# Kernel tuning notes

Hardware: AMD Instinct MI355X
Metric: run time of the kernel (lower is better)

## Reference

```python
import jax, jax.numpy as jnp
import numpy as np
import math

HIDDEN = 2048
HEADS = 16
GROUPS = 4
HEAD_DIM = HIDDEN // HEADS  # 128
KV_DIM = GROUPS * HEAD_DIM  # 512
B, S = 2, 2048


def setup_inputs() -> dict:
    key = jax.random.key(0)
    ks = jax.random.split(key, 10)
    scale = 0.02
    return {
        "X": jax.random.normal(ks[0], (B, S, HIDDEN), dtype=jnp.float32),
        "attention_mask": jnp.ones((B, S), dtype=jnp.int32),
        "Wq": jax.random.normal(ks[1], (HIDDEN, HIDDEN), dtype=jnp.float32) * scale,
        "bq": jnp.zeros((HIDDEN,), dtype=jnp.float32),
        "Wk": jax.random.normal(ks[2], (HIDDEN, KV_DIM), dtype=jnp.float32) * scale,
        "bk": jnp.zeros((KV_DIM,), dtype=jnp.float32),
        "Wv": jax.random.normal(ks[3], (HIDDEN, KV_DIM), dtype=jnp.float32) * scale,
        "bv": jnp.zeros((KV_DIM,), dtype=jnp.float32),
        "Wo": jax.random.normal(ks[4], (HIDDEN, HIDDEN), dtype=jnp.float32) * scale,
        "bo": jnp.zeros((HIDDEN,), dtype=jnp.float32),
    }


def reference(X, attention_mask, Wq, bq, Wk, bk, Wv, bv, Wo, bo):
    b, s, _ = X.shape
    num_per_group = HEADS // GROUPS
    # projections
    Q = (X @ Wq + bq).reshape(b, s, HEADS, HEAD_DIM).transpose(0, 2, 1, 3)   # [b,H,s,d]
    K = (X @ Wk + bk).reshape(b, s, GROUPS, HEAD_DIM).transpose(0, 2, 1, 3)  # [b,G,s,d]
    V = (X @ Wv + bv).reshape(b, s, GROUPS, HEAD_DIM).transpose(0, 2, 1, 3)
    # torch .repeat(1, num_per_group, 1, 1) tiles group axis: [g0..gG-1, g0..gG-1, ...]
    K = jnp.tile(K, (1, num_per_group, 1, 1))  # [b,H,s,d]
    V = jnp.tile(V, (1, num_per_group, 1, 1))
    scores = jnp.einsum("bhqd,bhkd->bhqk", Q, K) / math.sqrt(HEAD_DIM)
    mask = attention_mask[:, None, None, :] == 0  # [b,1,1,s]
    scores = jnp.where(mask, jnp.float32(-jnp.inf), scores)
    attn = jax.nn.softmax(scores, axis=-1)
    out = jnp.einsum("bhqk,bhkd->bhqd", attn, V)  # [b,H,s,d]
    out = out.transpose(0, 2, 1, 3).reshape(b, s, HIDDEN)
    return out @ Wo + bo
```

## Files before the change

kernel.cpp:

```cpp
#include <hip/hip_runtime.h>
#include <hip/hip_bf16.h>


typedef __attribute__((ext_vector_type(8))) short short8;
typedef __attribute__((ext_vector_type(4))) short short4v;
typedef __attribute__((ext_vector_type(4))) float float4v;
typedef __attribute__((ext_vector_type(16))) float float16v;

#define C1F 0.12751743f
#define B0F -16.0f

#if defined(__has_builtin) && __has_builtin(__builtin_amdgcn_exp2f)
#define EXP2(x) __builtin_amdgcn_exp2f(x)
#else
#define EXP2(x) exp2f(x)
#endif

__device__ __forceinline__ short f2bf(float x) {
    __hip_bfloat16 h = __float2bfloat16(x);
    short s; __builtin_memcpy(&s, &h, sizeof(s)); return s;
}

__device__ __forceinline__ void gl16(const short* g, short* l) {
    __builtin_amdgcn_global_load_lds(
        (const __attribute__((address_space(1))) void*)g,
        (__attribute__((address_space(3))) void*)l, 16, 0, 0);
}

__global__ __launch_bounds__(256) void prep_kernel(
    const float* __restrict__ X, short* __restrict__ Xb,
    const float* __restrict__ Wq, const float* __restrict__ Wk,
    const float* __restrict__ Wv, const float* __restrict__ Wo,
    short* __restrict__ WqkvT, short* __restrict__ Wot) {
    __shared__ float tile[32][33];
    const int bxg = blockIdx.x;
    if (bxg < 8192) {
        int i = (bxg * 256 + threadIdx.x) * 4;
        float4 v = *(const float4*)(X + i);
        short4v o;
        o[0] = f2bf(v.x); o[1] = f2bf(v.y); o[2] = f2bf(v.z); o[3] = f2bf(v.w);
        *(short4v*)(Xb + i) = o;
        return;
    }
    const int tid = bxg - 8192;
    int bx = tid % 160;
    const int k0 = (tid / 160) * 32;
    const float* W; short* Wt; int N;
    if (bx < 64)      { W = Wq; Wt = WqkvT;                      N = 2048; }
    else if (bx < 80) { W = Wk; Wt = WqkvT + (size_t)2048 * 2048; N = 512; bx -= 64; }
    else if (bx < 96) { W = Wv; Wt = WqkvT + (size_t)2560 * 2048; N = 512; bx -= 80; }
    else              { W = Wo; Wt = Wot;                        N = 2048; bx -= 96; }
    const int K = 2048;
    const int n0 = bx * 32;
    const int tx = threadIdx.x & 31, ty = threadIdx.x >> 5;
#pragma unroll
    for (int i = 0; i < 4; ++i) {
        int kk = ty + i * 8;
        tile[kk][tx] = W[(size_t)(k0 + kk) * N + n0 + tx];
    }
    __syncthreads();
#pragma unroll
    for (int i = 0; i < 4; ++i) {
        int nn = ty + i * 8;
        Wt[(size_t)(n0 + nn) * K + k0 + tx] = f2bf(tile[tx][nn]);
    }
}

__global__ __launch_bounds__(256) void gemm_dma_kernel(
    const short* __restrict__ A, const short* __restrict__ Bt,
    const float* __restrict__ b0, const float* __restrict__ b1, const float* __restrict__ b2,
    short* __restrict__ O0, short* __restrict__ O1, short* __restrict__ O2,
    float* __restrict__ Of, int K, int mode) {
    __shared__ short As[128 * 64];
    __shared__ short Bs[128 * 64];
    const int t = threadIdx.x, lane = t & 63, w = t >> 6;
    const int l15 = lane & 15, quad = lane >> 4;
    const int wm = (w & 1) * 64, wn = (w >> 1) * 64;
    const int m0 = blockIdx.y * 128, n0 = blockIdx.x * 128;
    const int r8 = lane >> 3;
    const int csw = ((lane & 7) ^ r8) * 8;
    const short* ga = A + (size_t)(m0 + w * 8 + r8) * K + csw;
    const short* gb = Bt + (size_t)(n0 + w * 8 + r8) * K + csw;
    short* lA = As + (w * 8) * 64;
    short* lB = Bs + (w * 8) * 64;
    const int xs = l15 & 7;

    float4v acc[4][4] = {};

    for (int k0 = 0; k0 < K; k0 += 64) {
#pragma unroll
        for (int c = 0; c < 4; ++c) {
            gl16(ga + k0 + (size_t)(c * 32) * K, lA + c * 2048);
            gl16(gb + k0 + (size_t)(c * 32) * K, lB + c * 2048);
        }
        __syncthreads();
#pragma unroll
        for (int ks = 0; ks < 2; ++ks) {
            short8 af[4], bfr[4];
            const int ps = ((ks * 4 + quad) ^ xs) * 8;
#pragma unroll
            for (int i = 0; i < 4; ++i)
                af[i] = *(const short8*)(As + (wm + i * 16 + l15) * 64 + ps);
#pragma unroll
            for (int j = 0; j < 4; ++j)
                bfr[j] = *(const short8*)(Bs + (wn + j * 16 + l15) * 64 + ps);
#pragma unroll
            for (int i = 0; i < 4; ++i)
#pragma unroll
                for (int j = 0; j < 4; ++j)
                    acc[i][j] = __builtin_amdgcn_mfma_f32_16x16x32_bf16(af[i], bfr[j], acc[i][j], 0, 0, 0);
        }
        __syncthreads();
    }

#pragma unroll
    for (int i = 0; i < 4; ++i) {
#pragma unroll
        for (int j = 0; j < 4; ++j) {
            const int col = n0 + wn + j * 16 + l15;
            const int row0 = m0 + wm + i * 16 + quad * 4;
            if (mode == 1) {
                const float bc = b0[col];
#pragma unroll
                for (int r = 0; r < 4; ++r)
                    Of[(size_t)(row0 + r) * 2048 + col] = acc[i][j][r] + bc;
            } else if (col < 2048) {
                const float bc = b0[col];
#pragma unroll
                for (int r = 0; r < 4; ++r)
                    O0[(size_t)(row0 + r) * 2048 + col] = f2bf(acc[i][j][r] + bc);
            } else if (col < 2560) {
                const int c = col - 2048;
                const float bc = b1[c];
#pragma unroll
                for (int r = 0; r < 4; ++r)
                    O1[(size_t)(row0 + r) * 512 + c] = f2bf(acc[i][j][r] + bc);
            } else {
                const int c = col - 2560;
                const float bc = b2[c];
                const int qsw = ((quad & 1) << 1) | (quad >> 1);
                const int prow = m0 + wm + i * 16 + qsw * 4;
#pragma unroll
                for (int r = 0; r < 4; ++r)
                    O2[(size_t)c * 4096 + prow + r] = f2bf(acc[i][j][r] + bc);
            }
        }
    }
}

__global__ __launch_bounds__(256, 2) void flash_kernel(
    const short* __restrict__ Qb, const short* __restrict__ Kb,
    const short* __restrict__ Vt, const int* __restrict__ mask,
    short* __restrict__ Ab) {
    __shared__ short Ks[2][64 * 136];
    __shared__ short Vs[2][128 * 72];

    const int t = threadIdx.x;
    const int lane = t & 63, w = t >> 6;
    const int l31 = lane & 31, hi = lane >> 5;
    const int qt = blockIdx.x, g = blockIdx.y, b = blockIdx.z;
    const int h = g + 4 * w;
    const int q0 = qt * 32;

    short8 qf[8];
#pragma unroll
    for (int dd = 0; dd < 8; ++dd)
        qf[dd] = *(const short8*)(Qb + (size_t)(b * 2048 + q0 + l31) * 2048
                                  + h * 128 + dd * 16 + hi * 8);

    float16v o[4] = {};
    float rsum = 0.f;

    const int kR = t >> 4, kC = (t & 15) * 8;
    const int vR = t >> 3, vC = (t & 7) * 8;
    const short* kg = Kb + (size_t)(b * 2048 + kR) * 512 + g * 128 + kC;
    const short* vg = Vt + (size_t)(g * 128 + vR) * 4096 + (size_t)b * 2048 + vC;

    short8 kv[4], vv[4];
    int mvr = 1;

#define LOADT(KB)                                                                  \
    do {                                                                           \
        kv[0] = *(const short8*)(kg + (size_t)(KB) * 512);                         \
        kv[1] = *(const short8*)(kg + (size_t)((KB) + 16) * 512);                  \
        kv[2] = *(const short8*)(kg + (size_t)((KB) + 32) * 512);                  \
        kv[3] = *(const short8*)(kg + (size_t)((KB) + 48) * 512);                  \
        vv[0] = *(const short8*)(vg + (KB));                                       \
        vv[1] = *(const short8*)(vg + (size_t)32 * 4096 + (KB));                   \
        vv[2] = *(const short8*)(vg + (size_t)64 * 4096 + (KB));                   \
        vv[3] = *(const short8*)(vg + (size_t)96 * 4096 + (KB));                   \
        mvr = mask[b * 2048 + (KB) + lane];                                        \
    } while (0)

#define STAGE(BUF)                                                                 \
    do {                                                                           \
        _Pragma("unroll")                                                          \
        for (int i_ = 0; i_ < 4; ++i_)                                             \
            *(short8*)(&Ks[BUF][(kR + i_ * 16) * 136 + kC]) = kv[i_];              \
        _Pragma("unroll")                                                          \
        for (int i_ = 0; i_ < 4; ++i_)                                             \
            *(short8*)(&Vs[BUF][(vR + i_ * 32) * 72 + vC]) = vv[i_];               \
    } while (0)

    LOADT(0);
    STAGE(0);
    unsigned long long bits = __ballot(mvr != 0);
    LOADT(64);
    __syncthreads();

    int cur = 0;
    unsigned long long bits_next = bits;

    for (int kt = 0; kt < 32; ++kt) {
        if (kt + 1 < 32) {
            STAGE(cur ^ 1);
            bits_next = __ballot(mvr != 0);
            if (kt + 2 < 32) LOADT((kt + 2) * 64);
        }
        const short* Ksb = &Ks[cur][0];
        const short* Vsb = &Vs[cur][0];

        float16v st0 = {}, st1 = {};
        __builtin_amdgcn_s_setprio(1);
#pragma unroll
        for (int dd = 0; dd < 8; ++dd) {
            short8 kf0 = *(const short8*)(Ksb + l31 * 136 + dd * 16 + hi * 8);
            short8 kf1 = *(const short8*)(Ksb + (32 + l31) * 136 + dd * 16 + hi * 8);
            st0 = __builtin_amdgcn_mfma_f32_32x32x16_bf16(kf0, qf[dd], st0, 0, 0, 0);
            st1 = __builtin_amdgcn_mfma_f32_32x32x16_bf16(kf1, qf[dd], st1, 0, 0, 0);
        }
        __builtin_amdgcn_s_setprio(0);

        const bool full = (bits == ~0ull);
        const unsigned int mlo = ((unsigned int)bits) >> (4 * hi);
        const unsigned int mhi = ((unsigned int)(bits >> 32)) >> (4 * hi);

        if (full) {
#pragma unroll
            for (int e = 0; e < 16; ++e) {
                float p0 = EXP2(fmaf(st0[e], C1F, B0F));
                rsum += p0; st0[e] = p0;
            }
        } else {
#pragma unroll
            for (int e = 0; e < 16; ++e) {
                const int koff = (e & 3) + 8 * (e >> 2);
                float p0 = EXP2(fmaf(st0[e], C1F, B0F));
                p0 = ((mlo >> koff) & 1) ? p0 : 0.f;
                rsum += p0; st0[e] = p0;
            }
        }

        __builtin_amdgcn_s_setprio(1);
#pragma unroll
        for (int cc = 0; cc < 2; ++cc) {
            short8 pa;
#pragma unroll
            for (int e = 0; e < 8; ++e) pa[e] = f2bf(st0[cc * 8 + e]);
#pragma unroll
            for (int db = 0; db < 4; ++db) {
                short8 vb = *(const short8*)(Vsb + (db * 32 + l31) * 72 + cc * 16 + hi * 8);
                o[db] = __builtin_amdgcn_mfma_f32_32x32x16_bf16(pa, vb, o[db], 0, 0, 0);
            }
        }
        __builtin_amdgcn_s_setprio(0);

        if (full) {
#pragma unroll
            for (int e = 0; e < 16; ++e) {
                float p1 = EXP2(fmaf(st1[e], C1F, B0F));
                rsum += p1; st1[e] = p1;
            }
        } else {
#pragma unroll
            for (int e = 0; e < 16; ++e) {
                const int koff = (e & 3) + 8 * (e >> 2);
                float p1 = EXP2(fmaf(st1[e], C1F, B0F));
                p1 = ((mhi >> koff) & 1) ? p1 : 0.f;
                rsum += p1; st1[e] = p1;
            }
        }

        __builtin_amdgcn_s_setprio(1);
#pragma unroll
        for (int cc = 2; cc < 4; ++cc) {
            short8 pa;
#pragma unroll
            for (int e = 0; e < 8; ++e) pa[e] = f2bf(st1[(cc & 1) * 8 + e]);
#pragma unroll
            for (int db = 0; db < 4; ++db) {
                short8 vb = *(const short8*)(Vsb + (db * 32 + l31) * 72 + cc * 16 + hi * 8);
                o[db] = __builtin_amdgcn_mfma_f32_32x32x16_bf16(pa, vb, o[db], 0, 0, 0);
            }
        }
        __builtin_amdgcn_s_setprio(0);

        __syncthreads();
        bits = bits_next;
        cur ^= 1;
    }
#undef LOADT
#undef STAGE

    rsum += __shfl_xor(rsum, 32, 64);
    const float rinv = (rsum > 0.f) ? 1.f / rsum : 0.f;
    float rq[16];
#pragma unroll
    for (int e = 0; e < 16; ++e) {
        const int koff = (e & 3) + 8 * (e >> 2);
        rq[e] = __shfl(rinv, koff + 4 * hi, 64);
    }
    const size_t ob = (size_t)(b * 2048 + q0) * 2048 + h * 128;
#pragma unroll
    for (int db = 0; db < 4; ++db)
#pragma unroll
        for (int e = 0; e < 16; ++e) {
            const int koff = (e & 3) + 8 * (e >> 2);
            Ab[ob + (size_t)(koff + 4 * hi) * 2048 + db * 32 + l31] =
                f2bf(o[db][e] * rq[e]);
        }
}

extern "C" void kernel_launch(void* const* d_in, const int* in_sizes, int n_in,
                              void* d_out, int out_size, void* d_ws, size_t ws_size,
                              hipStream_t stream) {
    (void)in_sizes; (void)n_in; (void)out_size; (void)ws_size;
    const float* X  = (const float*)d_in[0];
    const int* mask = (const int*)d_in[1];
    const float* Wq = (const float*)d_in[2];
    const float* bq = (const float*)d_in[3];
    const float* Wk = (const float*)d_in[4];
    const float* bk = (const float*)d_in[5];
    const float* Wv = (const float*)d_in[6];
    const float* bv = (const float*)d_in[7];
    const float* Wo = (const float*)d_in[8];
    const float* bo = (const float*)d_in[9];
    float* out = (float*)d_out;

    char* ws = (char*)d_ws;
    short* Xb     = (short*)(ws + 0);
    short* WqkvT  = (short*)(ws + 16777216);
    short* Wot    = (short*)(ws + 29360128);
    short* Qb     = (short*)(ws + 37748736);
    short* Kb     = (short*)(ws + 54525952);
    short* Vt     = (short*)(ws + 58720256);
    short* Ab     = Xb;

    const int HID = 2048;

    prep_kernel<<<18432, 256, 0, stream>>>(X, Xb, Wq, Wk, Wv, Wo, WqkvT, Wot);

    gemm_dma_kernel<<<dim3(24, 32), 256, 0, stream>>>(
        Xb, WqkvT, bq, bk, bv, Qb, Kb, Vt, nullptr, HID, 0);

    flash_kernel<<<dim3(64, 4, 2), 256, 0, stream>>>(Qb, Kb, Vt, mask, Ab);

    gemm_dma_kernel<<<dim3(16, 32), 256, 0, stream>>>(
        Ab, Wot, bo, nullptr, nullptr, nullptr, nullptr, nullptr, out, HID, 1);
}
```

Measured before the change: 304.8 us.

## Split flash attention KV tiles across two wave groups with LDS merge

```diff
diff --git a/kernel.cpp b/kernel.cpp
--- a/kernel.cpp
+++ b/kernel.cpp
@@ -148,18 +148,21 @@
     }
 }
 
-__global__ __launch_bounds__(256, 2) void flash_kernel(
+__global__ __launch_bounds__(512, 4) void flash_kernel(
     const short* __restrict__ Qb, const short* __restrict__ Kb,
     const short* __restrict__ Vt, const int* __restrict__ mask,
     short* __restrict__ Ab) {
-    __shared__ short Ks[2][64 * 136];
-    __shared__ short Vs[2][128 * 72];
+    __shared__ __align__(16) char smem[71680];
+    short* KsBase = (short*)smem;
+    short* VsBase = (short*)(smem + 34816);
+    float* mg = (float*)smem;
 
     const int t = threadIdx.x;
     const int lane = t & 63, w = t >> 6;
     const int l31 = lane & 31, hi = lane >> 5;
+    const int ksp = w >> 2;
     const int qt = blockIdx.x, g = blockIdx.y, b = blockIdx.z;
-    const int h = g + 4 * w;
+    const int h = g + 4 * (w & 3);
     const int q0 = qt * 32;
 
     short8 qf[8];
@@ -176,30 +179,26 @@
     const short* kg = Kb + (size_t)(b * 2048 + kR) * 512 + g * 128 + kC;
     const short* vg = Vt + (size_t)(g * 128 + vR) * 4096 + (size_t)b * 2048 + vC;
 
-    short8 kv[4], vv[4];
+    short8 kv[2], vv[2];
     int mvr = 1;
 
 #define LOADT(KB)                                                                  \
     do {                                                                           \
         kv[0] = *(const short8*)(kg + (size_t)(KB) * 512);                         \
-        kv[1] = *(const short8*)(kg + (size_t)((KB) + 16) * 512);                  \
-        kv[2] = *(const short8*)(kg + (size_t)((KB) + 32) * 512);                  \
-        kv[3] = *(const short8*)(kg + (size_t)((KB) + 48) * 512);                  \
+        kv[1] = *(const short8*)(kg + (size_t)((KB) + 32) * 512);                  \
         vv[0] = *(const short8*)(vg + (KB));                                       \
-        vv[1] = *(const short8*)(vg + (size_t)32 * 4096 + (KB));                   \
-        vv[2] = *(const short8*)(vg + (size_t)64 * 4096 + (KB));                   \
-        vv[3] = *(const short8*)(vg + (size_t)96 * 4096 + (KB));                   \
+        vv[1] = *(const short8*)(vg + (size_t)64 * 4096 + (KB));                   \
         mvr = mask[b * 2048 + (KB) + lane];                                        \
     } while (0)
 
 #define STAGE(BUF)                                                                 \
     do {                                                                           \
-        _Pragma("unroll")                                                          \
-        for (int i_ = 0; i_ < 4; ++i_)                                             \
-            *(short8*)(&Ks[BUF][(kR + i_ * 16) * 136 + kC]) = kv[i_];              \
-        _Pragma("unroll")                                                          \
-        for (int i_ = 0; i_ < 4; ++i_)                                             \
-            *(short8*)(&Vs[BUF][(vR + i_ * 32) * 72 + vC]) = vv[i_];               \
+        short* Ksw = KsBase + (BUF) * (64 * 136);                                  \
+        short* Vsw = VsBase + (BUF) * (128 * 72);                                  \
+        *(short8*)(Ksw + kR * 136 + kC) = kv[0];                                   \
+        *(short8*)(Ksw + (kR + 32) * 136 + kC) = kv[1];                            \
+        *(short8*)(Vsw + vR * 72 + vC) = vv[0];                                    \
+        *(short8*)(Vsw + (vR + 64) * 72 + vC) = vv[1];                             \
     } while (0)
 
     LOADT(0);
@@ -217,83 +216,81 @@
             bits_next = __ballot(mvr != 0);
             if (kt + 2 < 32) LOADT((kt + 2) * 64);
         }
-        const short* Ksb = &Ks[cur][0];
-        const short* Vsb = &Vs[cur][0];
-
-        float16v st0 = {}, st1 = {};
+        const short* Ksb = KsBase + cur * (64 * 136);
+        const short* Vsb = VsBase + cur * (128 * 72);
+
+        float16v st = {};
         __builtin_amdgcn_s_setprio(1);
 #pragma unroll
         for (int dd = 0; dd < 8; ++dd) {
-            short8 kf0 = *(const short8*)(Ksb + l31 * 136 + dd * 16 + hi * 8);
-            short8 kf1 = *(const short8*)(Ksb + (32 + l31) * 136 + dd * 16 + hi * 8);
-            st0 = __builtin_amdgcn_mfma_f32_32x32x16_bf16(kf0, qf[dd], st0, 0, 0, 0);
-            st1 = __builtin_amdgcn_mfma_f32_32x32x16_bf16(kf1, qf[dd], st1, 0, 0, 0);
+            short8 kf = *(const short8*)(Ksb + (ksp * 32 + l31) * 136 + dd * 16 + hi * 8);
+            st = __builtin_amdgcn_mfma_f32_32x32x16_bf16(kf, qf[dd], st, 0, 0, 0);
         }
         __builtin_amdgcn_s_setprio(0);
 
         const bool full = (bits == ~0ull);
-        const unsigned int mlo = ((unsigned int)bits) >> (4 * hi);
-        const unsigned int mhi = ((unsigned int)(bits >> 32)) >> (4 * hi);
+        const unsigned int mword =
+            (unsigned int)(ksp ? (bits >> 32) : bits) >> (4 * hi);
 
         if (full) {
 #pragma unroll
-            for (int e = 0; e < 16; ++e) {
-                float p0 = EXP2(fmaf(st0[e], C1F, B0F));
-                rsum += p0; st0[e] = p0;
+            for (int e = 0; e < 8; ++e) {
+                float p = EXP2(fmaf(st[e], C1F, B0F));
+                rsum += p; st[e] = p;
             }
         } else {
 #pragma unroll
-            for (int e = 0; e < 16; ++e) {
+            for (int e = 0; e < 8; ++e) {
                 const int koff = (e & 3) + 8 * (e >> 2);
-                float p0 = EXP2(fmaf(st0[e], C1F, B0F));
-                p0 = ((mlo >> koff) & 1) ? p0 : 0.f;
-                rsum += p0; st0[e] = p0;
-            }
-        }
-
-        __builtin_amdgcn_s_setprio(1);
-#pragma unroll
-        for (int cc = 0; cc < 2; ++cc) {
+                float p = EXP2(fmaf(st[e], C1F, B0F));
+                p = ((mword >> koff) & 1) ? p : 0.f;
+                rsum += p; st[e] = p;
+            }
+        }
+
+        {
+            const int cc = ksp * 2;
             short8 pa;
 #pragma unroll
-            for (int e = 0; e < 8; ++e) pa[e] = f2bf(st0[cc * 8 + e]);
+            for (int e = 0; e < 8; ++e) pa[e] = f2bf(st[e]);
+            __builtin_amdgcn_s_setprio(1);
 #pragma unroll
             for (int db = 0; db < 4; ++db) {
                 short8 vb = *(const short8*)(Vsb + (db * 32 + l31) * 72 + cc * 16 + hi * 8);
                 o[db] = __builtin_amdgcn_mfma_f32_32x32x16_bf16(pa, vb, o[db], 0, 0, 0);
             }
-        }
-        __builtin_amdgcn_s_setprio(0);
+            __builtin_amdgcn_s_setprio(0);
+        }
 
         if (full) {
 #pragma unroll
-            for (int e = 0; e < 16; ++e) {
-                float p1 = EXP2(fmaf(st1[e], C1F, B0F));
-                rsum += p1; st1[e] = p1;
+            for (int e = 8; e < 16; ++e) {
+                float p = EXP2(fmaf(st[e], C1F, B0F));
+                rsum += p; st[e] = p;
             }
         } else {
 #pragma unroll
-            for (int e = 0; e < 16; ++e) {
+            for (int e = 8; e < 16; ++e) {
                 const int koff = (e & 3) + 8 * (e >> 2);
-                float p1 = EXP2(fmaf(st1[e], C1F, B0F));
-                p1 = ((mhi >> koff) & 1) ? p1 : 0.f;
-                rsum += p1; st1[e] = p1;
-            }
-        }
-
-        __builtin_amdgcn_s_setprio(1);
-#pragma unroll
-        for (int cc = 2; cc < 4; ++cc) {
+                float p = EXP2(fmaf(st[e], C1F, B0F));
+                p = ((mword >> koff) & 1) ? p : 0.f;
+                rsum += p; st[e] = p;
+            }
+        }
+
+        {
+            const int cc = ksp * 2 + 1;
             short8 pa;
 #pragma unroll
-            for (int e = 0; e < 8; ++e) pa[e] = f2bf(st1[(cc & 1) * 8 + e]);
+            for (int e = 0; e < 8; ++e) pa[e] = f2bf(st[8 + e]);
+            __builtin_amdgcn_s_setprio(1);
 #pragma unroll
             for (int db = 0; db < 4; ++db) {
                 short8 vb = *(const short8*)(Vsb + (db * 32 + l31) * 72 + cc * 16 + hi * 8);
                 o[db] = __builtin_amdgcn_mfma_f32_32x32x16_bf16(pa, vb, o[db], 0, 0, 0);
             }
-        }
-        __builtin_amdgcn_s_setprio(0);
+            __builtin_amdgcn_s_setprio(0);
+        }
 
         __syncthreads();
         bits = bits_next;
@@ -303,22 +300,43 @@
 #undef STAGE
 
     rsum += __shfl_xor(rsum, 32, 64);
-    const float rinv = (rsum > 0.f) ? 1.f / rsum : 0.f;
-    float rq[16];
-#pragma unroll
-    for (int e = 0; e < 16; ++e) {
-        const int koff = (e & 3) + 8 * (e >> 2);
-        rq[e] = __shfl(rinv, koff + 4 * hi, 64);
-    }
-    const size_t ob = (size_t)(b * 2048 + q0) * 2048 + h * 128;
-#pragma unroll
-    for (int db = 0; db < 4; ++db)
+
+    if (w >= 4) {
+        const int base = (w - 4) * (64 * 65) + lane * 65;
+#pragma unroll
+        for (int db = 0; db < 4; ++db)
+#pragma unroll
+            for (int e = 0; e < 16; ++e)
+                mg[base + db * 16 + e] = o[db][e];
+        mg[base + 64] = rsum;
+    }
+    __syncthreads();
+    if (w < 4) {
+        const int base = w * (64 * 65) + lane * 65;
+#pragma unroll
+        for (int db = 0; db < 4; ++db)
+#pragma unroll
+            for (int e = 0; e < 16; ++e)
+                o[db][e] += mg[base + db * 16 + e];
+        rsum += mg[base + 64];
+
+        const float rinv = (rsum > 0.f) ? 1.f / rsum : 0.f;
+        float rq[16];
 #pragma unroll
         for (int e = 0; e < 16; ++e) {
             const int koff = (e & 3) + 8 * (e >> 2);
-            Ab[ob + (size_t)(koff + 4 * hi) * 2048 + db * 32 + l31] =
-                f2bf(o[db][e] * rq[e]);
-        }
+            rq[e] = __shfl(rinv, koff + 4 * hi, 64);
+        }
+        const size_t ob = (size_t)(b * 2048 + q0) * 2048 + h * 128;
+#pragma unroll
+        for (int db = 0; db < 4; ++db)
+#pragma unroll
+            for (int e = 0; e < 16; ++e) {
+                const int koff = (e & 3) + 8 * (e >> 2);
+                Ab[ob + (size_t)(koff + 4 * hi) * 2048 + db * 32 + l31] =
+                    f2bf(o[db][e] * rq[e]);
+            }
+    }
 }
 
 extern "C" void kernel_launch(void* const* d_in, const int* in_sizes, int n_in,
@@ -353,7 +371,7 @@
     gemm_dma_kernel<<<dim3(24, 32), 256, 0, stream>>>(
         Xb, WqkvT, bq, bk, bv, Qb, Kb, Vt, nullptr, HID, 0);
 
-    flash_kernel<<<dim3(64, 4, 2), 256, 0, stream>>>(Qb, Kb, Vt, mask, Ab);
+    flash_kernel<<<dim3(64, 4, 2), 512, 0, stream>>>(Qb, Kb, Vt, mask, Ab);
 
     gemm_dma_kernel<<<dim3(16, 32), 256, 0, stream>>>(
         Ab, Wot, bo, nullptr, nullptr, nullptr, nullptr, nullptr, out, HID, 1);
```

New measurement: 406.7 us. 33.4% more time.
